# Kernel optimization log

Hardware: AMD Instinct MI355X
Metric: run time of the kernel (lower is better)

## Reference

```python
import jax, jax.numpy as jnp
import numpy as np

T = 36
N_POLES = 40
LAM = 0.1
MAX_ITER = 100
TOL = 1e-4
B, P = 2, 4096


def build_dictionary(Drr, Dtheta):
    # rows i = 0..T-1; columns: [rr^i cos(i th), (-rr)^i cos(i th), rr^i sin(i th), (-rr)^i sin(i th)]
    i = jnp.arange(T, dtype=Drr.dtype)[:, None]              # [T,1]
    pr = jnp.power(Drr[None, :], i)                          # rr^i   [T,N]
    sign = jnp.power(jnp.asarray(-1.0, Drr.dtype), i)        # (-1)^i [T,1]
    c = jnp.cos(i * Dtheta[None, :])
    s = jnp.sin(i * Dtheta[None, :])
    dic = jnp.concatenate([pr * c, sign * pr * c, pr * s, sign * pr * s], axis=1)  # [T,4N]
    G = jnp.linalg.norm(dic, axis=0)                         # column norms
    G = jnp.where(G == 0, jnp.sqrt(jnp.asarray(float(T), dic.dtype)), G)
    return dic / G


def soft_shrink(v, lambd):
    return jnp.sign(v) * jnp.maximum(jnp.abs(v) - lambd, 0.0)


def fista(D, Y, lam, max_iter=MAX_ITER):
    DtD = D.T @ D                                            # [4N,4N]
    L = jnp.linalg.norm(DtD)                                 # torch.norm(DtD, 2) = Frobenius norm
    linv = 1.0 / L
    DtY = jnp.einsum('tk,btp->bkp', D, Y) * linv             # [B,4N,P]
    K = DtD.shape[0]
    A = jnp.eye(K, dtype=D.dtype) - DtD * linv               # [4N,4N]
    lambd = lam * linv
    Bb, _, Pp = DtY.shape

    # FISTA momentum coefficients are data independent -> precompute
    ts = np.ones(max_iter + 1)
    for k in range(max_iter):
        ts[k + 1] = (1 + np.sqrt(1 + 4 * ts[k] ** 2)) / 2.0
    tts = jnp.asarray((ts[:-1] - 1) / ts[1:], dtype=D.dtype)  # [max_iter]

    x0 = jnp.zeros((Bb, K, Pp), dtype=D.dtype)

    def step(carry, inputs):
        x_old, y_old, done = carry
        tt, k = inputs
        x_new = soft_shrink(jnp.einsum('kj,bjp->bkp', A, y_old) + DtY, lambd)
        y_new = x_new * (1 + tt) - x_old * tt
        # torch divides by x_old.shape[1]: P on the first check (x_old is the 2-D zeros init), 4N after
        denom = jnp.where(k == 0, float(Pp), float(K)).astype(x_new.dtype)
        conv = jnp.linalg.norm(x_old - x_new) / denom < TOL
        x_out = jnp.where(done, x_old, x_new)
        y_out = jnp.where(done, y_old, y_new)
        return (x_out, y_out, jnp.logical_or(done, conv)), None

    (x_fin, _, _), _ = jax.lax.scan(step, (x0, x0, jnp.array(False)),
                                    (tts, jnp.arange(max_iter)))
    return x_fin


def setup_inputs() -> dict:
    key = jax.random.key(0)
    k1, k2, k3 = jax.random.split(key, 3)
    Drr = jax.random.uniform(k1, (N_POLES,), dtype=jnp.float32)
    Dtheta = jax.random.uniform(k2, (N_POLES,), dtype=jnp.float32)
    x = jax.random.normal(k3, (B, T, P), dtype=jnp.float32)
    return {"Drr": Drr, "Dtheta": Dtheta, "x": x}


def reference(Drr, Dtheta, x):
    dic = build_dictionary(Drr, Dtheta)   # [T, 4N]
    sparsecode = fista(dic, x, LAM)       # [B, 4N, P]
    return sparsecode
```

## Files before the change

### kernel.cpp

```cpp
#include <hip/hip_runtime.h>
#include <hip/hip_fp16.h>
#include <cmath>

#define TT 36
#define KK 160
#define NPOLE 40
#define PP 4096
#define MAXIT 100
#define COLS 16
#define NG 2
#define NWC 4
#define NTHR 512
#define YS 168
#define GRID 256

typedef float    floatx4 __attribute__((ext_vector_type(4)));
typedef _Float16 halfx8  __attribute__((ext_vector_type(8)));

__device__ __align__(16) float    g_D[TT * KK];
__device__ __align__(16) float    g_rown[KK];
__device__ __align__(16) _Float16 g_A[KK * KK];

struct TtsArg { float v[MAXIT]; };

static TtsArg host_tts() {
  TtsArg a;
  double ts = 1.0;
  for (int k = 0; k < MAXIT; k++) {
    double tn = (1.0 + sqrt(1.0 + 4.0 * ts * ts)) * 0.5;
    a.v[k] = (float)((ts - 1.0) / tn);
    ts = tn;
  }
  return a;
}

__global__ __launch_bounds__(256)
void setup_kernel(const float* __restrict__ Drr, const float* __restrict__ Dth) {
  __shared__ float Dl[TT * KK];
  __shared__ float red[256];
  const int a = blockIdx.x, tid = threadIdx.x;

  if (tid < KK) {
    int gg = tid / NPOLE, n = tid % NPOLE;
    float rr = Drr[n], th = Dth[n];
    float srr = (gg & 1) ? -rr : rr;
    float sth, cth; __sincosf(th, &sth, &cth);
    float c = 1.f, s = 0.f, pr = 1.f, ss = 0.f;
    for (int t = 0; t < TT; t++) {
      float val = pr * ((gg < 2) ? c : s);
      Dl[t * KK + tid] = val;
      ss = fmaf(val, val, ss);
      float cn = c * cth - s * sth;
      float sn = s * cth + c * sth;
      c = cn; s = sn; pr *= srr;
    }
    float gn = sqrtf(ss);
    gn = (gn == 0.f) ? sqrtf((float)TT) : gn;
    float inv = 1.f / gn;
    for (int t = 0; t < TT; t++) Dl[t * KK + tid] *= inv;
  }
  __syncthreads();

  if (a == 0)
    for (int idx = tid; idx < TT * KK; idx += 256) g_D[idx] = Dl[idx];

  float ss2 = 0.f;
  if (tid < KK) {
    float s2 = 0.f;
    for (int t = 0; t < TT; t++) s2 = fmaf(Dl[t * KK + a], Dl[t * KK + tid], s2);
    g_A[a * KK + tid] = (_Float16)((tid == a) ? 0.f : s2);
    ss2 = s2 * s2;
  }
  red[tid] = ss2;
  __syncthreads();
  for (int off = 128; off > 0; off >>= 1) {
    if (tid < off) red[tid] += red[tid + off];
    __syncthreads();
  }
  if (tid == 0) g_rown[a] = red[0];
}

__global__ __launch_bounds__(NTHR, 2)
void fista_kernel(const float* __restrict__ x, float* __restrict__ out,
                  TtsArg targ) {
  __shared__ __align__(16) short ys[NG][2][COLS * YS];
  __shared__ float ttsl[MAXIT];
  __shared__ unsigned cnt[NG];

  const int tid  = threadIdx.x;
  const int w    = tid >> 6;
  const int lane = tid & 63;
  const int quad = lane >> 4;
  const int l16  = lane & 15;
  const int g    = w >> 2;
  const int v    = w & 3;
  const int bid  = blockIdx.x;
  const int bb   = (bid * 32) / PP;
  const int p0   = (bid * 32) % PP + 16 * g;

  float frob = 0.f;
#pragma unroll
  for (int i = 0; i < KK; i += 4) {
    float4 r4 = *(const float4*)&g_rown[i];
    frob += ((r4.x + r4.y) + r4.z) + r4.w;
  }
  const float linv  = 1.0f / sqrtf(frob);
  const float nlinv = -linv;
  const float lambd = 0.1f * linv;
  const float adiag = 1.0f - linv;

  int base, nrs;
  if (g == 0) { base = (v < 2) ? 48 * v : 32 * v + 32; nrs = (v < 2) ? 3 : 2; }
  else        { base = (v < 2) ? 32 * v : 48 * v - 32; nrs = (v < 2) ? 2 : 3; }

  for (int i = tid; i < MAXIT; i += NTHR) ttsl[i] = targ.v[i];

  halfx8 ah[3][5];
#pragma unroll
  for (int rs = 0; rs < 3; rs++) {
    if (rs < nrs) {
      const int myrow = base + 16 * rs + l16;
#pragma unroll
      for (int kc = 0; kc < 5; kc++)
        ah[rs][kc] = *(const halfx8*)&g_A[myrow * KK + 32 * kc + 8 * quad];
    }
  }

  float dty[3][4] = {{0.f,0.f,0.f,0.f},{0.f,0.f,0.f,0.f},{0.f,0.f,0.f,0.f}};
  {
    const float* xcol = &x[(size_t)bb * TT * PP + p0 + l16];
    for (int t = 0; t < TT; t++) {
      float xv = xcol[(size_t)t * PP];
#pragma unroll
      for (int rs = 0; rs < 3; rs++) {
        if (rs < nrs) {
          float4 d = *(const float4*)&g_D[t * KK + base + 16 * rs + 4 * quad];
          dty[rs][0] = fmaf(d.x, xv, dty[rs][0]);
          dty[rs][1] = fmaf(d.y, xv, dty[rs][1]);
          dty[rs][2] = fmaf(d.z, xv, dty[rs][2]);
          dty[rs][3] = fmaf(d.w, xv, dty[rs][3]);
        }
      }
    }
#pragma unroll
    for (int rs = 0; rs < 3; rs++)
#pragma unroll
      for (int r = 0; r < 4; r++) dty[rs][r] = -dty[rs][r];
  }

  {
    int* z = (int*)&ys[0][0][0];
    for (int i = tid; i < NG * 2 * COLS * YS / 2; i += NTHR) z[i] = 0;
    if (tid < NG) cnt[tid] = 0;
  }
  float xo[3][4] = {{0.f,0.f,0.f,0.f},{0.f,0.f,0.f,0.f},{0.f,0.f,0.f,0.f}};
  float yv[3][4] = {{0.f,0.f,0.f,0.f},{0.f,0.f,0.f,0.f},{0.f,0.f,0.f,0.f}};
  __syncthreads();

  if (g == 1) __builtin_amdgcn_s_sleep(10);
  __builtin_amdgcn_s_setprio(1);

#define RD_MFMA(KC) { \
    halfx8 bh = *(const halfx8*)&yb[cb + 32 * (KC)]; \
    _Pragma("unroll") \
    for (int rs = 0; rs < 3; rs++) \
      if (rs < nrs) \
        accM[rs] = __builtin_amdgcn_mfma_f32_16x16x32_f16(ah[rs][KC], bh, accM[rs], 0, 0, 0); \
  }

#define ITER_BODY(SK, K1, K2, K3, K4) { \
    RD_MFMA(SK) \
    if (it > 0) { \
      const unsigned tgt = (unsigned)(NWC * it); \
      __builtin_amdgcn_s_setprio(0); \
      while (__atomic_load_n(&cnt[g], __ATOMIC_ACQUIRE) < tgt) \
        __builtin_amdgcn_s_sleep(1); \
      __builtin_amdgcn_s_setprio(1); \
    } \
    RD_MFMA(K1) RD_MFMA(K2) RD_MFMA(K3) RD_MFMA(K4) \
  }

  for (int it = 0; it < MAXIT; it++) {
    const short* yb = &ys[g][it & 1][0];
    const int cb = l16 * YS + 8 * quad;
    floatx4 accM[3] = {{dty[0][0], dty[0][1], dty[0][2], dty[0][3]},
                       {dty[1][0], dty[1][1], dty[1][2], dty[1][3]},
                       {dty[2][0], dty[2][1], dty[2][2], dty[2][3]}};

    if (g == 0) {
      if      (v == 0) ITER_BODY(0, 1, 2, 3, 4)
      else if (v == 1) ITER_BODY(2, 0, 1, 3, 4)
      else if (v == 2) ITER_BODY(3, 0, 1, 2, 4)
      else             ITER_BODY(4, 0, 1, 2, 3)
    } else {
      if      (v == 0) ITER_BODY(0, 1, 2, 3, 4)
      else if (v == 1) ITER_BODY(1, 0, 2, 3, 4)
      else if (v == 2) ITER_BODY(2, 0, 1, 3, 4)
      else             ITER_BODY(4, 0, 1, 2, 3)
    }

    const float tt = ttsl[it];
    short* yw = &ys[g][(it & 1) ^ 1][0];
#pragma unroll
    for (int rs = 0; rs < 3; rs++) {
      if (rs < nrs) {
        float yn[4];
#pragma unroll
        for (int r = 0; r < 4; r++) {
          float vv = fmaf(nlinv, accM[rs][r], adiag * yv[rs][r]);
          float cl = __builtin_amdgcn_fmed3f(vv, -lambd, lambd);
          float xv = vv - cl;
          yn[r] = fmaf(tt, xv - xo[rs][r], xv);
          xo[rs][r] = xv;
          yv[rs][r] = yn[r];
        }
        _Float16 h0 = (_Float16)yn[0], h1 = (_Float16)yn[1];
        _Float16 h2 = (_Float16)yn[2], h3 = (_Float16)yn[3];
        unsigned u01 = (unsigned)__builtin_bit_cast(unsigned short, h0) |
                       ((unsigned)__builtin_bit_cast(unsigned short, h1) << 16);
        unsigned u23 = (unsigned)__builtin_bit_cast(unsigned short, h2) |
                       ((unsigned)__builtin_bit_cast(unsigned short, h3) << 16);
        const int ko = l16 * YS + base + 16 * rs + 4 * quad;
        *(uint2*)&yw[ko] = make_uint2(u01, u23);
      }
    }

    if (lane == 0) __atomic_fetch_add(&cnt[g], 1u, __ATOMIC_RELEASE);
  }

#pragma unroll
  for (int rs = 0; rs < 3; rs++) {
    if (rs < nrs) {
#pragma unroll
      for (int r = 0; r < 4; r++)
        out[((size_t)bb * KK + base + 16 * rs + 4 * quad + r) * PP + p0 + l16] = xo[rs][r];
    }
  }
}

extern "C" void kernel_launch(void* const* d_in, const int* in_sizes, int n_in,
                              void* d_out, int out_size, void* d_ws, size_t ws_size,
                              hipStream_t stream) {
  const float* Drr = (const float*)d_in[0];
  const float* Dth = (const float*)d_in[1];
  const float* x   = (const float*)d_in[2];
  float* out = (float*)d_out;
  (void)d_ws; (void)ws_size; (void)in_sizes; (void)n_in; (void)out_size;

  setup_kernel<<<160, 256, 0, stream>>>(Drr, Dth);
  fista_kernel<<<GRID, NTHR, 0, stream>>>(x, out, host_tts());
}
```

Before: 152.8 us.

## Split each column group across eight waves with finer row-slice assignment

Doubles the block to 1024 threads so each 16-column group is handled by 8 waves instead of 4. Each wave now owns one or two 16-row slices instead of two or three, which shortens the per-wave MFMA chain on the critical path of each FISTA iteration. Waves whose rows fall in a k-chunk they wrote themselves keep the early self-chunk MFMA before the wait; the others wait first and then run all five chunks. The trade-off is more waves contending on the shared counter spin-wait and more synchronisation overhead per iteration.

```diff
diff --git a/kernel.cpp b/kernel.cpp
--- a/kernel.cpp
+++ b/kernel.cpp
@@ -9,8 +9,8 @@
 #define MAXIT 100
 #define COLS 16
 #define NG 2
-#define NWC 4
-#define NTHR 512
+#define NWC 8
+#define NTHR 1024
 #define YS 168
 #define GRID 256
 
@@ -80,7 +80,7 @@
   if (tid == 0) g_rown[a] = red[0];
 }
 
-__global__ __launch_bounds__(NTHR, 2)
+__global__ __launch_bounds__(NTHR, 4)
 void fista_kernel(const float* __restrict__ x, float* __restrict__ out,
                   TtsArg targ) {
   __shared__ __align__(16) short ys[NG][2][COLS * YS];
@@ -92,8 +92,8 @@
   const int lane = tid & 63;
   const int quad = lane >> 4;
   const int l16  = lane & 15;
-  const int g    = w >> 2;
-  const int v    = w & 3;
+  const int g    = w >> 3;
+  const int v    = w & 7;
   const int bid  = blockIdx.x;
   const int bb   = (bid * 32) / PP;
   const int p0   = (bid * 32) % PP + 16 * g;
@@ -110,14 +110,14 @@
   const float adiag = 1.0f - linv;
 
   int base, nrs;
-  if (g == 0) { base = (v < 2) ? 48 * v : 32 * v + 32; nrs = (v < 2) ? 3 : 2; }
-  else        { base = (v < 2) ? 32 * v : 48 * v - 32; nrs = (v < 2) ? 2 : 3; }
+  if (g == 0) { base = (v < 6) ? 16 * v : 32 * v - 96; nrs = (v < 6) ? 1 : 2; }
+  else        { base = (v < 2) ? 32 * v : 16 * v + 32; nrs = (v < 2) ? 2 : 1; }
 
   for (int i = tid; i < MAXIT; i += NTHR) ttsl[i] = targ.v[i];
 
-  halfx8 ah[3][5];
-#pragma unroll
-  for (int rs = 0; rs < 3; rs++) {
+  halfx8 ah[2][5];
+#pragma unroll
+  for (int rs = 0; rs < 2; rs++) {
     if (rs < nrs) {
       const int myrow = base + 16 * rs + l16;
 #pragma unroll
@@ -126,13 +126,13 @@
     }
   }
 
-  float dty[3][4] = {{0.f,0.f,0.f,0.f},{0.f,0.f,0.f,0.f},{0.f,0.f,0.f,0.f}};
+  float dty[2][4] = {{0.f,0.f,0.f,0.f},{0.f,0.f,0.f,0.f}};
   {
     const float* xcol = &x[(size_t)bb * TT * PP + p0 + l16];
     for (int t = 0; t < TT; t++) {
       float xv = xcol[(size_t)t * PP];
 #pragma unroll
-      for (int rs = 0; rs < 3; rs++) {
+      for (int rs = 0; rs < 2; rs++) {
         if (rs < nrs) {
           float4 d = *(const float4*)&g_D[t * KK + base + 16 * rs + 4 * quad];
           dty[rs][0] = fmaf(d.x, xv, dty[rs][0]);
@@ -143,7 +143,7 @@
       }
     }
 #pragma unroll
-    for (int rs = 0; rs < 3; rs++)
+    for (int rs = 0; rs < 2; rs++)
 #pragma unroll
       for (int r = 0; r < 4; r++) dty[rs][r] = -dty[rs][r];
   }
@@ -153,8 +153,8 @@
     for (int i = tid; i < NG * 2 * COLS * YS / 2; i += NTHR) z[i] = 0;
     if (tid < NG) cnt[tid] = 0;
   }
-  float xo[3][4] = {{0.f,0.f,0.f,0.f},{0.f,0.f,0.f,0.f},{0.f,0.f,0.f,0.f}};
-  float yv[3][4] = {{0.f,0.f,0.f,0.f},{0.f,0.f,0.f,0.f},{0.f,0.f,0.f,0.f}};
+  float xo[2][4] = {{0.f,0.f,0.f,0.f},{0.f,0.f,0.f,0.f}};
+  float yv[2][4] = {{0.f,0.f,0.f,0.f},{0.f,0.f,0.f,0.f}};
   __syncthreads();
 
   if (g == 1) __builtin_amdgcn_s_sleep(10);
@@ -163,13 +163,12 @@
 #define RD_MFMA(KC) { \
     halfx8 bh = *(const halfx8*)&yb[cb + 32 * (KC)]; \
     _Pragma("unroll") \
-    for (int rs = 0; rs < 3; rs++) \
+    for (int rs = 0; rs < 2; rs++) \
       if (rs < nrs) \
         accM[rs] = __builtin_amdgcn_mfma_f32_16x16x32_f16(ah[rs][KC], bh, accM[rs], 0, 0, 0); \
   }
 
-#define ITER_BODY(SK, K1, K2, K3, K4) { \
-    RD_MFMA(SK) \
+#define WAIT_ONCE { \
     if (it > 0) { \
       const unsigned tgt = (unsigned)(NWC * it); \
       __builtin_amdgcn_s_setprio(0); \
@@ -177,32 +176,39 @@
         __builtin_amdgcn_s_sleep(1); \
       __builtin_amdgcn_s_setprio(1); \
     } \
+  }
+
+#define ITER_SELF(SK, K1, K2, K3, K4) { \
+    RD_MFMA(SK) \
+    WAIT_ONCE \
     RD_MFMA(K1) RD_MFMA(K2) RD_MFMA(K3) RD_MFMA(K4) \
+  }
+
+#define ITER_PLAIN { \
+    WAIT_ONCE \
+    RD_MFMA(0) RD_MFMA(1) RD_MFMA(2) RD_MFMA(3) RD_MFMA(4) \
   }
 
   for (int it = 0; it < MAXIT; it++) {
     const short* yb = &ys[g][it & 1][0];
     const int cb = l16 * YS + 8 * quad;
-    floatx4 accM[3] = {{dty[0][0], dty[0][1], dty[0][2], dty[0][3]},
-                       {dty[1][0], dty[1][1], dty[1][2], dty[1][3]},
-                       {dty[2][0], dty[2][1], dty[2][2], dty[2][3]}};
+    floatx4 accM[2] = {{dty[0][0], dty[0][1], dty[0][2], dty[0][3]},
+                       {dty[1][0], dty[1][1], dty[1][2], dty[1][3]}};
 
     if (g == 0) {
-      if      (v == 0) ITER_BODY(0, 1, 2, 3, 4)
-      else if (v == 1) ITER_BODY(2, 0, 1, 3, 4)
-      else if (v == 2) ITER_BODY(3, 0, 1, 2, 4)
-      else             ITER_BODY(4, 0, 1, 2, 3)
+      if      (v == 6) ITER_SELF(3, 0, 1, 2, 4)
+      else if (v == 7) ITER_SELF(4, 0, 1, 2, 3)
+      else             ITER_PLAIN
     } else {
-      if      (v == 0) ITER_BODY(0, 1, 2, 3, 4)
-      else if (v == 1) ITER_BODY(1, 0, 2, 3, 4)
-      else if (v == 2) ITER_BODY(2, 0, 1, 3, 4)
-      else             ITER_BODY(4, 0, 1, 2, 3)
+      if      (v == 0) ITER_SELF(0, 1, 2, 3, 4)
+      else if (v == 1) ITER_SELF(1, 0, 2, 3, 4)
+      else             ITER_PLAIN
     }
 
     const float tt = ttsl[it];
     short* yw = &ys[g][(it & 1) ^ 1][0];
 #pragma unroll
-    for (int rs = 0; rs < 3; rs++) {
+    for (int rs = 0; rs < 2; rs++) {
       if (rs < nrs) {
         float yn[4];
 #pragma unroll
@@ -229,7 +235,7 @@
   }
 
 #pragma unroll
-  for (int rs = 0; rs < 3; rs++) {
+  for (int rs = 0; rs < 2; rs++) {
     if (rs < nrs) {
 #pragma unroll
       for (int r = 0; r < 4; r++)
```

After: 220.7 us. 44.4% more time.
